# Performance work log

Hardware: AMD Instinct MI355X
Metric: run time of the kernel (lower is better)

The kernel has to match this reference:

```python
import jax, jax.numpy as jnp
import numpy as np

V = 50000      # vocabulary size (len(negative_sampling_table))
E = 256        # embedding_size
R = 180        # time_scope_radius -> 2R+1 = 361 time buckets
B = 2048       # batch
L = 200        # context length
NOPT = 10      # number of candidate targets (mixed_target has NOPT+1 cols)


def setup_inputs() -> dict:
    key = jax.random.key(0)
    k1, k2, k3, k4, k5, k6 = jax.random.split(key, 6)
    context = jax.random.randint(k1, (B, L, 2), 0, V, dtype=jnp.int64)
    mixed_target = jax.random.randint(k2, (B, NOPT + 1), 0, V, dtype=jnp.int64)
    context_emb_table = jax.random.normal(k3, (V, E), dtype=jnp.float32)
    target_emb_table = jax.random.normal(k4, (V, E), dtype=jnp.float32)
    taa_matrix = jax.random.uniform(k5, (V, 2 * R + 1), dtype=jnp.float32)
    taa_bias = jax.random.uniform(k6, (V, 1), dtype=jnp.float32)
    return {
        "context": context,
        "mixed_target": mixed_target,
        "context_emb_table": context_emb_table,
        "target_emb_table": target_emb_table,
        "taa_matrix": taa_matrix,
        "taa_bias": taa_bias,
    }


def reference(context, mixed_target, context_emb_table, target_emb_table, taa_matrix, taa_bias):
    radius = (taa_matrix.shape[1] - 1) // 2
    context_event = context[:, :, 0]          # [B, L]
    context_time = context[:, :, 1]           # [B, L]
    n_options = mixed_target.shape[-1] - 1
    target_event = mixed_target[:, :n_options]   # [B, n_options]
    target_time = mixed_target[:, n_options:]    # [B, 1]

    # mask padded positions (event id == -1)
    context_mask = jnp.where(context_event == -1, 0, 1)
    context_event = context_event * context_mask

    context_embedding = context_emb_table[context_event]          # [B, L, E]

    time_delta = jnp.clip(context_time - target_time + radius, 0, 2 * radius)  # [B, L]

    activated_taa = jax.nn.softmax(taa_matrix + taa_bias, axis=1)  # [V, 2R+1]
    taa_weights = activated_taa[context_event, time_delta]         # [B, L]

    # weighted masked sum over context positions
    w = taa_weights * context_mask.astype(taa_weights.dtype)       # [B, L]
    hidden = jnp.einsum("ble,bl->be", context_embedding, w)       # [B, E]

    target_embedding = target_emb_table[target_event]              # [B, n_options, E]
    scores = jnp.einsum("bne,be->bn", target_embedding, hidden)   # [B, n_options]
    return scores
```

## Files before the change

### kernel.cpp

```cpp
#include <hip/hip_runtime.h>
#include <hip/hip_bf16.h>

#define V 50000
#define E 256
#define RADIUS 180
#define TAA_W (2 * RADIUS + 1)
#define BATCH 2048
#define CTX_L 200
#define NOPT 10

#define ISE_BLOCKS  (V / 16)
#define CONV_BLOCKS 3125
#define CONV_STRIDE (CONV_BLOCKS * 256)

typedef float vf4 __attribute__((ext_vector_type(4)));

__device__ __forceinline__ unsigned short f2bf_rne(float f) {
    unsigned u = __float_as_uint(f);
    u += 0x7fffu + ((u >> 16) & 1u);
    return (unsigned short)(u >> 16);
}
__device__ __forceinline__ unsigned pack_bf16(float a, float b) {
    return (unsigned)f2bf_rne(a) | ((unsigned)f2bf_rne(b) << 16);
}
__device__ __forceinline__ float bf_lo(unsigned u) {
    return __uint_as_float(u << 16);
}
__device__ __forceinline__ float bf_hi(unsigned u) {
    return __uint_as_float(u & 0xffff0000u);
}

__global__ __launch_bounds__(256) void prep_fused_kernel(
    const float* __restrict__ taa, const float* __restrict__ ctx_tab,
    float* __restrict__ inv, uint2* __restrict__ btab, int do_conv)
{
    __shared__ float s_e[16 * TAA_W];
    const int tid = threadIdx.x;
    const int blk = blockIdx.x;
    if (blk < ISE_BLOCKS) {
        const float4* p = (const float4*)taa + (size_t)blk * 1444;
#pragma unroll
        for (int k = 0; k < 6; ++k) {
            int j = tid + 256 * k;
            if (j < 1444) {
                float4 v = p[j];
                float* d = &s_e[4 * j];
                d[0] = __expf(v.x);
                d[1] = __expf(v.y);
                d[2] = __expf(v.z);
                d[3] = __expf(v.w);
            }
        }
        __syncthreads();
        const int r = tid >> 4;
        const int c = tid & 15;
        const float* row = &s_e[r * TAA_W];
        float s = 0.f;
#pragma unroll
        for (int i = c; i < TAA_W; i += 16) s += row[i];
        for (int off = 1; off < 16; off <<= 1) s += __shfl_xor(s, off, 64);
        if (c == 0) inv[16 * blk + r] = 1.0f / s;
    } else if (do_conv) {
        const vf4* src = (const vf4*)ctx_tab;
        size_t base = (size_t)(blk - ISE_BLOCKS) * 256 + tid;
#pragma unroll
        for (int r = 0; r < 4; ++r) {
            size_t i = base + (size_t)r * CONV_STRIDE;
            vf4 v = __builtin_nontemporal_load(src + i);
            uint2 o;
            o.x = pack_bf16(v.x, v.y);
            o.y = pack_bf16(v.z, v.w);
            btab[i] = o;
        }
    }
}

template <int USE_BF16>
__global__ __launch_bounds__(256) void mce_taa_main_kernel(
    const int*   __restrict__ ctx,
    const int*   __restrict__ mt,
    const float* __restrict__ ctx_tab,
    const uint2* __restrict__ btab,
    const float* __restrict__ tgt_tab,
    const float* __restrict__ taa,
    const float* __restrict__ inv,
    float*       __restrict__ out)
{
    __shared__ int   s_ev[CTX_L];
    __shared__ float s_w[CTX_L];
    __shared__ float s_part[4 * E];
    __shared__ float s_hid[E];

    const int b   = blockIdx.x;
    const int tid = threadIdx.x;
    const int tgt_time = mt[b * (NOPT + 1) + NOPT];

    if (tid < CTX_L) {
        int2 ct = ((const int2*)ctx)[b * CTX_L + tid];
        int ev = ct.x, t = ct.y;
        int mask = (ev == -1) ? 0 : 1;
        ev = mask ? ev : 0;
        if (ev < 0) ev += V;
        int td = t - tgt_time + RADIUS;
        td = min(max(td, 0), 2 * RADIUS);
        float x = taa[(size_t)ev * TAA_W + td];
        s_ev[tid] = ev;
        s_w[tid]  = mask ? __expf(x) * inv[ev] : 0.f;
    }
    __syncthreads();

    const int ws   = tid >> 6;
    const int lane = tid & 63;

    float a0 = 0.f, a1 = 0.f, a2 = 0.f, a3 = 0.f;
    if (USE_BF16) {
#pragma unroll 3
        for (int l0 = 0; l0 < 192; l0 += 16) {
            int   la = l0 + ws,      lb = l0 + 4 + ws;
            int   lc = l0 + 8 + ws,  ld = l0 + 12 + ws;
            int   ea = s_ev[la], eb = s_ev[lb], ec = s_ev[lc], ed = s_ev[ld];
            float wa = s_w[la],  wb = s_w[lb],  wc = s_w[lc],  wd = s_w[ld];
            uint2 ua = btab[(size_t)ea * (E / 4) + lane];
            uint2 ub = btab[(size_t)eb * (E / 4) + lane];
            uint2 uc = btab[(size_t)ec * (E / 4) + lane];
            uint2 ud = btab[(size_t)ed * (E / 4) + lane];
            a0 = fmaf(bf_lo(ua.x), wa, a0);
            a1 = fmaf(bf_hi(ua.x), wa, a1);
            a2 = fmaf(bf_lo(ua.y), wa, a2);
            a3 = fmaf(bf_hi(ua.y), wa, a3);
            a0 = fmaf(bf_lo(ub.x), wb, a0);
            a1 = fmaf(bf_hi(ub.x), wb, a1);
            a2 = fmaf(bf_lo(ub.y), wb, a2);
            a3 = fmaf(bf_hi(ub.y), wb, a3);
            a0 = fmaf(bf_lo(uc.x), wc, a0);
            a1 = fmaf(bf_hi(uc.x), wc, a1);
            a2 = fmaf(bf_lo(uc.y), wc, a2);
            a3 = fmaf(bf_hi(uc.y), wc, a3);
            a0 = fmaf(bf_lo(ud.x), wd, a0);
            a1 = fmaf(bf_hi(ud.x), wd, a1);
            a2 = fmaf(bf_lo(ud.y), wd, a2);
            a3 = fmaf(bf_hi(ud.y), wd, a3);
        }
        {
            int   la = 192 + ws,     lb = 196 + ws;
            int   ea = s_ev[la],     eb = s_ev[lb];
            float wa = s_w[la],      wb = s_w[lb];
            uint2 ua = btab[(size_t)ea * (E / 4) + lane];
            uint2 ub = btab[(size_t)eb * (E / 4) + lane];
            a0 = fmaf(bf_lo(ua.x), wa, a0);
            a1 = fmaf(bf_hi(ua.x), wa, a1);
            a2 = fmaf(bf_lo(ua.y), wa, a2);
            a3 = fmaf(bf_hi(ua.y), wa, a3);
            a0 = fmaf(bf_lo(ub.x), wb, a0);
            a1 = fmaf(bf_hi(ub.x), wb, a1);
            a2 = fmaf(bf_lo(ub.y), wb, a2);
            a3 = fmaf(bf_hi(ub.y), wb, a3);
        }
    } else {
        const float4* tab4 = (const float4*)ctx_tab;
#pragma unroll 5
        for (int l0 = 0; l0 < CTX_L; l0 += 4) {
            int    l  = l0 + ws;
            int    ev = s_ev[l];
            float  w  = s_w[l];
            float4 u  = tab4[(size_t)ev * (E / 4) + lane];
            a0 = fmaf(u.x, w, a0);
            a1 = fmaf(u.y, w, a1);
            a2 = fmaf(u.z, w, a2);
            a3 = fmaf(u.w, w, a3);
        }
    }
    {
        float* p = &s_part[ws * E + lane * 4];
        p[0] = a0; p[1] = a1; p[2] = a2; p[3] = a3;
    }
    __syncthreads();
    s_hid[tid] = s_part[tid] + s_part[E + tid] + s_part[2 * E + tid] + s_part[3 * E + tid];
    __syncthreads();

    const float4* ttab4 = (const float4*)tgt_tab;
    for (int n = ws; n < NOPT; n += 4) {
        int tg = mt[b * (NOPT + 1) + n];
        if (tg < 0) tg += V;
        float4 u = ttab4[(size_t)tg * (E / 4) + lane];
        float p = u.x * s_hid[lane * 4 + 0]
                + u.y * s_hid[lane * 4 + 1]
                + u.z * s_hid[lane * 4 + 2]
                + u.w * s_hid[lane * 4 + 3];
        for (int off = 32; off > 0; off >>= 1) p += __shfl_xor(p, off, 64);
        if (lane == 0) out[b * NOPT + n] = p;
    }
}

extern "C" void kernel_launch(void* const* d_in, const int* in_sizes, int n_in,
                              void* d_out, int out_size, void* d_ws, size_t ws_size,
                              hipStream_t stream) {
    const int*   ctx     = (const int*)d_in[0];
    const int*   mt      = (const int*)d_in[1];
    const float* ctx_tab = (const float*)d_in[2];
    const float* tgt_tab = (const float*)d_in[3];
    const float* taa     = (const float*)d_in[4];
    float* out = (float*)d_out;

    float* inv  = (float*)d_ws;
    uint2* btab = (uint2*)((char*)d_ws + (256 << 10));
    const size_t need = (256 << 10) + (size_t)V * E * 2;
    const int use_bf16 = (ws_size >= need) ? 1 : 0;

    prep_fused_kernel<<<ISE_BLOCKS + (use_bf16 ? CONV_BLOCKS : 0), 256, 0,
                        stream>>>(taa, ctx_tab, inv, btab, use_bf16);
    if (use_bf16) {
        mce_taa_main_kernel<1><<<BATCH, 256, 0, stream>>>(
            ctx, mt, ctx_tab, btab, tgt_tab, taa, inv, out);
    } else {
        mce_taa_main_kernel<0><<<BATCH, 256, 0, stream>>>(
            ctx, mt, ctx_tab, btab, tgt_tab, taa, inv, out);
    }
}
```

Before: 216.0 us.

## Make prep kernel persistent with grid-stride softmax-sum and bf16 conversion loops

Replaces the one-block-per-work-item prep kernel (3125 softmax-denominator blocks plus 3125 conversion blocks) with a fixed 2048-block persistent grid. Each block loops over 8-row groups to compute the inverse softmax sums and then grid-strides over the context table to convert it to bf16, two vectors per iteration. The aim is to cut block launch and scheduling overhead and to let one block overlap the two phases. The cost is an extra barrier per group and smaller per-group work, with the row-sum reduction now spread over 32 lanes.

```diff
diff --git a/kernel.cpp b/kernel.cpp
--- a/kernel.cpp
+++ b/kernel.cpp
@@ -9,9 +9,9 @@
 #define CTX_L 200
 #define NOPT 10
 
-#define ISE_BLOCKS  (V / 16)
-#define CONV_BLOCKS 3125
-#define CONV_STRIDE (CONV_BLOCKS * 256)
+#define ISE_GROUPS (V / 8)
+#define VEC4_TOTAL (V * E / 4)
+#define PREP_GRID  2048
 
 typedef float vf4 __attribute__((ext_vector_type(4)));
 
@@ -30,19 +30,19 @@
     return __uint_as_float(u & 0xffff0000u);
 }
 
-__global__ __launch_bounds__(256) void prep_fused_kernel(
+__global__ __launch_bounds__(256) void prep_persist_kernel(
     const float* __restrict__ taa, const float* __restrict__ ctx_tab,
     float* __restrict__ inv, uint2* __restrict__ btab, int do_conv)
 {
-    __shared__ float s_e[16 * TAA_W];
+    __shared__ float s_e[8 * TAA_W];
     const int tid = threadIdx.x;
-    const int blk = blockIdx.x;
-    if (blk < ISE_BLOCKS) {
-        const float4* p = (const float4*)taa + (size_t)blk * 1444;
+
+    for (int g = blockIdx.x; g < ISE_GROUPS; g += PREP_GRID) {
+        const float4* p = (const float4*)taa + (size_t)g * 722;
 #pragma unroll
-        for (int k = 0; k < 6; ++k) {
+        for (int k = 0; k < 3; ++k) {
             int j = tid + 256 * k;
-            if (j < 1444) {
+            if (j < 722) {
                 float4 v = p[j];
                 float* d = &s_e[4 * j];
                 d[0] = __expf(v.x);
@@ -52,20 +52,33 @@
             }
         }
         __syncthreads();
-        const int r = tid >> 4;
-        const int c = tid & 15;
+        const int r = tid >> 5;
+        const int c = tid & 31;
         const float* row = &s_e[r * TAA_W];
         float s = 0.f;
 #pragma unroll
-        for (int i = c; i < TAA_W; i += 16) s += row[i];
-        for (int off = 1; off < 16; off <<= 1) s += __shfl_xor(s, off, 64);
-        if (c == 0) inv[16 * blk + r] = 1.0f / s;
-    } else if (do_conv) {
+        for (int i = c; i < TAA_W; i += 32) s += row[i];
+        for (int off = 1; off < 32; off <<= 1) s += __shfl_xor(s, off, 64);
+        if (c == 0) inv[8 * g + r] = 1.0f / s;
+        __syncthreads();
+    }
+
+    if (do_conv) {
         const vf4* src = (const vf4*)ctx_tab;
-        size_t base = (size_t)(blk - ISE_BLOCKS) * 256 + tid;
-#pragma unroll
-        for (int r = 0; r < 4; ++r) {
-            size_t i = base + (size_t)r * CONV_STRIDE;
+        size_t i = (size_t)blockIdx.x * 256 + tid;
+        const size_t step = (size_t)PREP_GRID * 256;
+        for (; i + step < VEC4_TOTAL; i += 2 * step) {
+            vf4 va = __builtin_nontemporal_load(src + i);
+            vf4 vb = __builtin_nontemporal_load(src + i + step);
+            uint2 oa, ob;
+            oa.x = pack_bf16(va.x, va.y);
+            oa.y = pack_bf16(va.z, va.w);
+            ob.x = pack_bf16(vb.x, vb.y);
+            ob.y = pack_bf16(vb.z, vb.w);
+            btab[i] = oa;
+            btab[i + step] = ob;
+        }
+        if (i < VEC4_TOTAL) {
             vf4 v = __builtin_nontemporal_load(src + i);
             uint2 o;
             o.x = pack_bf16(v.x, v.y);
@@ -207,8 +220,8 @@
     const size_t need = (256 << 10) + (size_t)V * E * 2;
     const int use_bf16 = (ws_size >= need) ? 1 : 0;
 
-    prep_fused_kernel<<<ISE_BLOCKS + (use_bf16 ? CONV_BLOCKS : 0), 256, 0,
-                        stream>>>(taa, ctx_tab, inv, btab, use_bf16);
+    prep_persist_kernel<<<PREP_GRID, 256, 0, stream>>>(taa, ctx_tab, inv, btab,
+                                                       use_bf16);
     if (use_bf16) {
         mce_taa_main_kernel<1><<<BATCH, 256, 0, stream>>>(
             ctx, mt, ctx_tab, btab, tgt_tab, taa, inv, out);
```

New measurement: 214.6 us. No clear change (-0.6%).
